# Kernel optimization log

Hardware: AMD Instinct MI355X
Metric: run time of the kernel (lower is better)

Reference implementation:

```python
import jax, jax.numpy as jnp
import numpy as np
import math

B, S, H, NH = 2, 2048, 1024, 16
DK = H // NH
EPS = 1e-5

def setup_inputs() -> dict:
    key = jax.random.key(0)
    ks = jax.random.split(key, 8)
    sd = 0.02
    return {
        "x": jax.random.normal(ks[0], (B, S, H), dtype=jnp.float32),
        "ln1_w": jnp.ones((H,), jnp.float32),
        "ln1_b": jnp.zeros((H,), jnp.float32),
        "W_qkv": jax.random.normal(ks[1], (H, 3 * H), jnp.float32) * sd,
        "b_qkv": jnp.zeros((3 * H,), jnp.float32),
        "W_o": jax.random.normal(ks[2], (H, H), jnp.float32) * sd,
        "b_o": jnp.zeros((H,), jnp.float32),
        "ln2_w": jnp.ones((H,), jnp.float32),
        "ln2_b": jnp.zeros((H,), jnp.float32),
        "W_fc": jax.random.normal(ks[3], (H, 4 * H), jnp.float32) * sd,
        "b_fc": jnp.zeros((4 * H,), jnp.float32),
        "W_proj": jax.random.normal(ks[4], (4 * H, H), jnp.float32) * sd,
        "b_proj": jnp.zeros((H,), jnp.float32),
    }

def _layernorm(x, w, b):
    mu = jnp.mean(x, axis=-1, keepdims=True)
    var = jnp.mean(jnp.square(x - mu), axis=-1, keepdims=True)
    return (x - mu) * jax.lax.rsqrt(var + EPS) * w + b

def _attn(x, W_qkv, b_qkv, W_o, b_o):
    bs, seq, _ = x.shape
    qkv = x @ W_qkv + b_qkv                      # [b,s,3H]
    q, k, v = jnp.split(qkv, 3, axis=-1)
    q = q.reshape(bs, seq, NH, DK).transpose(0, 2, 1, 3)  # [b,h,s,d]
    k = k.reshape(bs, seq, NH, DK).transpose(0, 2, 1, 3)
    v = v.reshape(bs, seq, NH, DK).transpose(0, 2, 1, 3)
    scores = jnp.einsum("bhqd,bhkd->bhqk", q, k) / math.sqrt(DK)
    causal = jnp.tril(jnp.ones((seq, seq), bool))
    scores = jnp.where(causal, scores, -jnp.inf)
    attn = jax.nn.softmax(scores, axis=-1)
    out = jnp.einsum("bhqk,bhkd->bhqd", attn, v)
    out = out.transpose(0, 2, 1, 3).reshape(bs, seq, H)
    return out @ W_o + b_o

def reference(x, ln1_w, ln1_b, W_qkv, b_qkv, W_o, b_o, ln2_w, ln2_b, W_fc, b_fc, W_proj, b_proj):
    x = x + _attn(_layernorm(x, ln1_w, ln1_b), W_qkv, b_qkv, W_o, b_o)
    h = _layernorm(x, ln2_w, ln2_b)
    h = jax.nn.gelu(h @ W_fc + b_fc, approximate=False) @ W_proj + b_proj
    return x + h
```

## Files before the change

### kernel.cpp

```cpp
#include <hip/hip_runtime.h>
#include <hip/hip_bf16.h>
#include <math.h>

#define H_DIM 1024
#define SEQ   2048
#define BATCH 2
#define NHEAD 16
#define DKV   64
#define ROWS  (BATCH*SEQ)
#define QSCALE 0.18033688f

typedef __attribute__((ext_vector_type(8))) short short8;
typedef __attribute__((ext_vector_type(4))) float f32x4;

static __device__ __forceinline__ unsigned short f32_bf16(float f) {
    unsigned int u = __builtin_bit_cast(unsigned int, f);
    u += 0x7FFF + ((u >> 16) & 1);
    return (unsigned short)(u >> 16);
}
static __device__ __forceinline__ float bf16_f32(unsigned short h) {
    return __builtin_bit_cast(float, (unsigned int)h << 16);
}

static __device__ __forceinline__ float fast_erf(float x) {
    float ax = fabsf(x);
    float t = 1.0f / fmaf(0.3275911f, ax, 1.0f);
    float p = t * fmaf(t, fmaf(t, fmaf(t, fmaf(t, 1.061405429f, -1.453152027f),
                                       1.421413741f), -0.284496736f), 0.254829592f);
    float y = fmaf(-p, __expf(-ax * ax), 1.0f);
    return copysignf(y, x);
}

static __device__ __forceinline__ void gload16(const unsigned short* g, unsigned short* l) {
    __builtin_amdgcn_global_load_lds(
        (const __attribute__((address_space(1))) void*)g,
        (__attribute__((address_space(3))) void*)l,
        16, 0, 0);
}

__global__ __launch_bounds__(256) void transpose_bf16(const float* __restrict__ in,
                                                      unsigned short* __restrict__ out,
                                                      int K, int N) {
    __shared__ float tile[32][33];
    int n0 = blockIdx.x * 32, k0 = blockIdx.y * 32;
    int tx = threadIdx.x & 31, ty = threadIdx.x >> 5;
    #pragma unroll
    for (int i = 0; i < 4; ++i)
        tile[ty + i * 8][tx] = in[(size_t)(k0 + ty + i * 8) * N + n0 + tx];
    __syncthreads();
    #pragma unroll
    for (int i = 0; i < 4; ++i)
        out[(size_t)(n0 + ty + i * 8) * K + k0 + tx] = f32_bf16(tile[tx][ty + i * 8]);
}

template<int BF16IN>
__global__ __launch_bounds__(256) void ln_any(const void* __restrict__ xin,
                                              const float* __restrict__ w,
                                              const float* __restrict__ bb,
                                              unsigned short* __restrict__ out) {
    int row = blockIdx.x;
    int tid = threadIdx.x;
    float4 v;
    if (BF16IN) {
        ushort4 u = ((const ushort4*)((const unsigned short*)xin + (size_t)row * H_DIM))[tid];
        v.x = bf16_f32(u.x); v.y = bf16_f32(u.y); v.z = bf16_f32(u.z); v.w = bf16_f32(u.w);
    } else {
        v = ((const float4*)((const float*)xin + (size_t)row * H_DIM))[tid];
    }
    float s  = v.x + v.y + v.z + v.w;
    float s2 = v.x*v.x + v.y*v.y + v.z*v.z + v.w*v.w;
    #pragma unroll
    for (int off = 1; off < 64; off <<= 1) {
        s  += __shfl_xor(s,  off, 64);
        s2 += __shfl_xor(s2, off, 64);
    }
    __shared__ float red[8];
    int wv = tid >> 6;
    if ((tid & 63) == 0) { red[wv] = s; red[4 + wv] = s2; }
    __syncthreads();
    s  = red[0] + red[1] + red[2] + red[3];
    s2 = red[4] + red[5] + red[6] + red[7];
    float mu = s * (1.0f / H_DIM);
    float rs = rsqrtf(s2 * (1.0f / H_DIM) - mu * mu + 1e-5f);
    float4 wv4 = ((const float4*)w)[tid];
    float4 bv4 = ((const float4*)bb)[tid];
    ushort4 o;
    o.x = f32_bf16((v.x - mu) * rs * wv4.x + bv4.x);
    o.y = f32_bf16((v.y - mu) * rs * wv4.y + bv4.y);
    o.z = f32_bf16((v.z - mu) * rs * wv4.z + bv4.z);
    o.w = f32_bf16((v.w - mu) * rs * wv4.w + bv4.w);
    ((ushort4*)(out + (size_t)row * H_DIM))[tid] = o;
}

template<int EPI>
static __device__ __forceinline__ void epi_store(f32x4 a, int row0, int col, int N,
                                                 const float* __restrict__ bias,
                                                 const float* __restrict__ resid,
                                                 float* __restrict__ outF,
                                                 unsigned short* __restrict__ outH,
                                                 unsigned short* __restrict__ outH2) {
    float bv = bias[col];
    if (EPI == 4 && col >= 2048) {
        int bb = row0 >> 11, ss = row0 & 2047;
        int hd = col - 2048;
        ushort4 u;
        u.x = f32_bf16(a[0] + bv);
        u.y = f32_bf16(a[1] + bv);
        u.z = f32_bf16(a[2] + bv);
        u.w = f32_bf16(a[3] + bv);
        *(ushort4*)&outH2[((size_t)bb * 1024 + hd) * SEQ + ss] = u;
    } else {
        #pragma unroll
        for (int j = 0; j < 4; ++j) {
            int row = row0 + j;
            size_t idx = (size_t)row * N + col;
            float c = a[j] + bv;
            if (EPI == 0) {
                outF[idx] = c;
            } else if (EPI == 1) {
                outF[idx] = resid[idx] + c;
            } else if (EPI == 2) {
                float g = 0.5f * c * (1.0f + fast_erf(c * 0.70710678118f));
                outH[idx] = f32_bf16(g);
            } else if (EPI == 3) {
                outH[idx] = f32_bf16(c);
            } else if (EPI == 5) {
                outH[idx] = f32_bf16(resid[idx] + c);
            } else if (EPI == 6) {
                outF[idx] = bf16_f32(outH2[idx]) + c;
            } else {
                float c2 = (col < 1024) ? c * QSCALE : c;
                outH[(size_t)row * 2048 + col] = f32_bf16(c2);
            }
        }
    }
}

template<int EPI, int NI>
__global__ __launch_bounds__(512) void gemmT(const unsigned short* __restrict__ A,
                                             const unsigned short* __restrict__ Bt,
                                             const float* __restrict__ bias,
                                             const float* __restrict__ resid,
                                             float* __restrict__ outF,
                                             unsigned short* __restrict__ outH,
                                             unsigned short* __restrict__ outH2,
                                             int gx, int N, int K) {
    constexpr int BN = NI * 32;
    constexpr int WN = BN / 4;
    constexpr int NT = WN / 16;
    __shared__ __attribute__((aligned(16))) unsigned short As[128][64];
    __shared__ __attribute__((aligned(16))) unsigned short Bs[BN][64];
    int tid = threadIdx.x;
    int w = tid >> 6, l = tid & 63;
    int l15 = l & 15, lg = l >> 4;
    int wm = w & 1, wn = w >> 1;

    int qq = gridDim.x >> 3;
    int wg = (blockIdx.x & 7) * qq + (blockIdx.x >> 3);
    int bm = wg / gx, bn = wg - bm * gx;
    int m0 = bm * 128, n0 = bn * BN;

    f32x4 acc[4][NT] = {};

    const unsigned short* aptr[2];
    unsigned short* lA[2];
    #pragma unroll
    for (int j = 0; j < 2; ++j) {
        int slot = j * 512 + tid;
        int row = slot >> 3;
        int lchunk = (slot & 7) ^ (row & 7);
        aptr[j] = A + (size_t)(m0 + row) * K + lchunk * 8;
        lA[j] = &As[0][0] + (size_t)slot * 8 - l * 8;
    }
    const unsigned short* bptr[NI / 2];
    unsigned short* lB[NI / 2];
    #pragma unroll
    for (int j = 0; j < NI / 2; ++j) {
        int slot = j * 512 + tid;
        int row = slot >> 3;
        int lchunk = (slot & 7) ^ (row & 7);
        bptr[j] = Bt + (size_t)(n0 + row) * K + lchunk * 8;
        lB[j] = &Bs[0][0] + (size_t)slot * 8 - l * 8;
    }
    int swz[2];
    swz[0] = ((0 + lg) ^ (l15 & 7)) * 8;
    swz[1] = ((4 + lg) ^ (l15 & 7)) * 8;
    const unsigned short* pA = &As[wm * 64 + l15][0];
    const unsigned short* pB = &Bs[wn * WN + l15][0];

    for (int k0 = 0; k0 < K; k0 += 64) {
        __syncthreads();
        #pragma unroll
        for (int j = 0; j < 2; ++j) gload16(aptr[j] + k0, lA[j]);
        #pragma unroll
        for (int j = 0; j < NI / 2; ++j) gload16(bptr[j] + k0, lB[j]);
        __syncthreads();

        #pragma unroll
        for (int ks = 0; ks < 2; ++ks) {
            short8 af[4], bf[NT];
            #pragma unroll
            for (int mi = 0; mi < 4; ++mi)
                af[mi] = *(const short8*)(pA + mi * 16 * 64 + swz[ks]);
            #pragma unroll
            for (int ni = 0; ni < NT; ++ni)
                bf[ni] = *(const short8*)(pB + ni * 16 * 64 + swz[ks]);
            #pragma unroll
            for (int mi = 0; mi < 4; ++mi)
                #pragma unroll
                for (int ni = 0; ni < NT; ++ni)
                    acc[mi][ni] = __builtin_amdgcn_mfma_f32_16x16x32_bf16(af[mi], bf[ni], acc[mi][ni], 0, 0, 0);
        }
    }

    #pragma unroll
    for (int mi = 0; mi < 4; ++mi)
        #pragma unroll
        for (int ni = 0; ni < NT; ++ni)
            epi_store<EPI>(acc[mi][ni], m0 + wm * 64 + mi * 16 + lg * 4,
                           n0 + wn * WN + ni * 16 + l15, N, bias, resid, outF, outH, outH2);
}

__global__ __launch_bounds__(512) void attn_mfma(const unsigned short* __restrict__ qk,
                                                 const unsigned short* __restrict__ vT,
                                                 unsigned short* __restrict__ out) {
    int bid = blockIdx.x;
    int swz = (bid & 7) * 64 + (bid >> 3);
    int b  = swz >> 8;
    int h  = (swz >> 4) & 15;
    int qt = 15 - (swz & 15);
    int tid = threadIdx.x;
    int w = tid >> 6, l = tid & 63;
    int l15 = l & 15, lg = l >> 4;

    __shared__ __attribute__((aligned(16))) unsigned short Ks[2][64][64];
    __shared__ __attribute__((aligned(16))) unsigned short Vt[2][64][64];
    __shared__ __attribute__((aligned(16))) unsigned short Ps[8][16][72];

    int qrow = qt * 128 + w * 16 + l15;
    short8 qf[2];
    {
        const unsigned short* qp = qk + (size_t)(b * SEQ + qrow) * 2048 + h * DKV + lg * 8;
        qf[0] = *(const short8*)qp;
        qf[1] = *(const short8*)(qp + 32);
    }
    short8 vf5;
    #pragma unroll
    for (int i = 0; i < 8; ++i) vf5[i] = (l15 == 0) ? (short)0x3F80 : (short)0;

    int srow = tid >> 3;
    int scl  = (tid & 7) * 8;
    int spc  = (((tid & 7) ^ (srow & 7)) * 8);
    const unsigned short* kbase = qk + (size_t)(b * SEQ + srow) * 2048 + 1024 + h * DKV + scl;
    const unsigned short* vbase = vT + ((size_t)(b * NHEAD + h) * DKV + srow) * SEQ + scl;

    int rk0 = ((0 * 4 + lg) ^ (l15 & 7)) * 8;
    int rk1 = ((1 * 4 + lg) ^ (l15 & 7)) * 8;

    float m = -1e30f;
    f32x4 oacc[4] = {};
    f32x4 oext = {};

    int nt = 2 * qt + 2;

    short8 kr0 = *(const short8*)kbase;
    short8 vr0 = *(const short8*)vbase;
    *(short8*)&Ks[0][srow][spc] = kr0;
    *(short8*)&Vt[0][srow][spc] = vr0;
    short8 kr1 = *(const short8*)(kbase + (size_t)64 * 2048);
    short8 vr1 = *(const short8*)(vbase + 64);
    __syncthreads();

#define ATTN_COMPUTE(BUF, KT)                                                          \
    {                                                                                  \
        f32x4 sc[4] = {};                                                              \
        __builtin_amdgcn_s_setprio(1);                                                 \
        _Pragma("unroll")                                                              \
        for (int st = 0; st < 4; ++st) {                                               \
            short8 kf0 = *(const short8*)&Ks[BUF][st * 16 + l15][rk0];                 \
            sc[st] = __builtin_amdgcn_mfma_f32_16x16x32_bf16(kf0, qf[0], sc[st], 0, 0, 0); \
            short8 kf1 = *(const short8*)&Ks[BUF][st * 16 + l15][rk1];                 \
            sc[st] = __builtin_amdgcn_mfma_f32_16x16x32_bf16(kf1, qf[1], sc[st], 0, 0, 0); \
        }                                                                              \
        __builtin_amdgcn_s_setprio(0);                                                 \
        float pv[4][4];                                                                \
        float pmax = -1e30f;                                                           \
        bool needmask = ((KT) * 64 + 63) > (qt * 128 + w * 16);      \
        if (needmask) {                                                                \
            int klim = qrow - (KT) * 64;                                               \
            _Pragma("unroll")                                                          \
            for (int st = 0; st < 4; ++st) {                                           \
                _Pragma("unroll")                                                      \
                for (int j = 0; j < 4; ++j) {                                          \
                    float s = sc[st][j];                                               \
                    if (st * 16 + lg * 4 + j > klim) s = -1e30f;                       \
                    pv[st][j] = s;                                                     \
                    pmax = fmaxf(pmax, s);                                             \
                }                                                                      \
            }                                                                          \
        } else {                                                                       \
            _Pragma("unroll")                                                          \
            for (int st = 0; st < 4; ++st) {                                           \
                _Pragma("unroll")                                                      \
                for (int j = 0; j < 4; ++j) {                                          \
                    pv[st][j] = sc[st][j];                                             \
                    pmax = fmaxf(pmax, sc[st][j]);                                     \
                }                                                                      \
            }                                                                          \
        }                                                                              \
        if (!__all(pmax - m <= 8.0f)) {                                                \
            float pr = fmaxf(pmax, __shfl_xor(pmax, 16, 64));                          \
            pr = fmaxf(pr, __shfl_xor(pr, 32, 64));                                    \
            float mn = fmaxf(m, pr);                                                   \
            float scl2 = exp2f(m - mn);                                                \
            _Pragma("unroll")                                                          \
            for (int d = 0; d < 4; ++d)                                                \
                _Pragma("unroll")                                                      \
                for (int j = 0; j < 4; ++j)                                            \
                    oacc[d][j] *= scl2;                                                \
            _Pragma("unroll")                                                          \
            for (int j = 0; j < 4; ++j) oext[j] *= scl2;                               \
            m = mn;                                                                    \
        }                                                                              \
        _Pragma("unroll")                                                              \
        for (int st = 0; st < 4; ++st) {                                               \
            float p0 = exp2f(pv[st][0] - m);                                           \
            float p1 = exp2f(pv[st][1] - m);                                           \
            float p2 = exp2f(pv[st][2] - m);                                           \
            float p3 = exp2f(pv[st][3] - m);                                           \
            unsigned int ua, ub;                                                       \
            asm("v_cvt_pk_bf16_f32 %0, %1, %2" : "=v"(ua) : "v"(p0), "v"(p1));         \
            asm("v_cvt_pk_bf16_f32 %0, %1, %2" : "=v"(ub) : "v"(p2), "v"(p3));         \
            uint2 u = make_uint2(ua, ub);                                              \
            *(uint2*)&Ps[w][l15][st * 16 + lg * 4] = u;                                \
        }                                                                              \
        __builtin_amdgcn_s_setprio(1);                                                 \
        _Pragma("unroll")                                                              \
        for (int ks = 0; ks < 2; ++ks) {                                               \
            short8 pf = *(const short8*)&Ps[w][l15][ks * 32 + lg * 8];                 \
            int rv = (ks == 0) ? rk0 : rk1;                                            \
            _Pragma("unroll")                                                          \
            for (int d = 0; d < 4; ++d) {                                              \
                short8 vf = *(const short8*)&Vt[BUF][d * 16 + l15][rv];                \
                oacc[d] = __builtin_amdgcn_mfma_f32_16x16x32_bf16(vf, pf, oacc[d], 0, 0, 0); \
            }                                                                          \
            oext = __builtin_amdgcn_mfma_f32_16x16x32_bf16(vf5, pf, oext, 0, 0, 0);    \
        }                                                                              \
        __builtin_amdgcn_s_setprio(0);                                                 \
    }

    for (int t = 0; t < nt; t += 2) {
        *(short8*)&Ks[1][srow][spc] = kr1;
        *(short8*)&Vt[1][srow][spc] = vr1;
        if (t + 2 < nt) {
            kr0 = *(const short8*)(kbase + (size_t)(t + 2) * 64 * 2048);
            vr0 = *(const short8*)(vbase + (t + 2) * 64);
        }
        ATTN_COMPUTE(0, t);
        __syncthreads();
        if (t + 2 < nt) {
            *(short8*)&Ks[0][srow][spc] = kr0;
            *(short8*)&Vt[0][srow][spc] = vr0;
            kr1 = *(const short8*)(kbase + (size_t)(t + 3) * 64 * 2048);
            vr1 = *(const short8*)(vbase + (t + 3) * 64);
        }
        ATTN_COMPUTE(1, t + 1);
        __syncthreads();
    }
#undef ATTN_COMPUTE

    float lsum = __shfl(oext[0], l15, 64);
    float inv = 1.0f / lsum;
    size_t ob = (size_t)(b * SEQ + qrow) * H_DIM + h * DKV;
    #pragma unroll
    for (int d = 0; d < 4; ++d) {
        ushort4 u;
        #pragma unroll
        for (int j = 0; j < 4; ++j)
            ((unsigned short*)&u)[j] = f32_bf16(oacc[d][j] * inv);
        *(ushort4*)&out[ob + d * 16 + lg * 4] = u;
    }
}

extern "C" void kernel_launch(void* const* d_in, const int* in_sizes, int n_in,
                              void* d_out, int out_size, void* d_ws, size_t ws_size,
                              hipStream_t stream) {
    const float* x     = (const float*)d_in[0];
    const float* ln1w  = (const float*)d_in[1];
    const float* ln1b  = (const float*)d_in[2];
    const float* Wqkv  = (const float*)d_in[3];
    const float* bqkv  = (const float*)d_in[4];
    const float* Wo    = (const float*)d_in[5];
    const float* bo    = (const float*)d_in[6];
    const float* ln2w  = (const float*)d_in[7];
    const float* ln2b  = (const float*)d_in[8];
    const float* Wfc   = (const float*)d_in[9];
    const float* bfc   = (const float*)d_in[10];
    const float* Wproj = (const float*)d_in[11];
    const float* bproj = (const float*)d_in[12];
    float* out = (float*)d_out;

    char* ws = (char*)d_ws;
    size_t off = 0;
    auto take = [&](size_t bytes) {
        void* p = ws + off;
        off += (bytes + 255) & ~(size_t)255;
        return p;
    };

    unsigned short* WqT  = (unsigned short*)take((size_t)3072 * 1024 * 2);
    unsigned short* WoT  = (unsigned short*)take((size_t)1024 * 1024 * 2);
    unsigned short* WfcT = (unsigned short*)take((size_t)4096 * 1024 * 2);
    unsigned short* WpT  = (unsigned short*)take((size_t)1024 * 4096 * 2);
    unsigned short* xn1   = (unsigned short*)take((size_t)ROWS * 1024 * 2);
    unsigned short* qk_h  = (unsigned short*)take((size_t)ROWS * 2048 * 2);
    unsigned short* vT    = (unsigned short*)take((size_t)ROWS * 1024 * 2);
    unsigned short* attn  = (unsigned short*)take((size_t)ROWS * 1024 * 2);
    unsigned short* x1h   = (unsigned short*)take((size_t)ROWS * 1024 * 2);
    unsigned short* xn2   = (unsigned short*)take((size_t)ROWS * 1024 * 2);
    unsigned short* hbuf  = (unsigned short*)take((size_t)ROWS * 4096 * 2);

    transpose_bf16<<<dim3(3072 / 32, 1024 / 32), 256, 0, stream>>>(Wqkv,  WqT,  1024, 3072);
    transpose_bf16<<<dim3(1024 / 32, 1024 / 32), 256, 0, stream>>>(Wo,    WoT,  1024, 1024);
    transpose_bf16<<<dim3(4096 / 32, 1024 / 32), 256, 0, stream>>>(Wfc,   WfcT, 1024, 4096);
    transpose_bf16<<<dim3(1024 / 32, 4096 / 32), 256, 0, stream>>>(Wproj, WpT,  4096, 1024);

    ln_any<0><<<ROWS, 256, 0, stream>>>(x, ln1w, ln1b, xn1);

    gemmT<4, 4><<<768, 512, 0, stream>>>(xn1, WqT, bqkv, nullptr, nullptr, qk_h, vT, 24, 3072, 1024);

    attn_mfma<<<512, 512, 0, stream>>>(qk_h, vT, attn);

    gemmT<5, 2><<<512, 512, 0, stream>>>(attn, WoT, bo, x, nullptr, x1h, nullptr, 16, 1024, 1024);

    ln_any<1><<<ROWS, 256, 0, stream>>>(x1h, ln2w, ln2b, xn2);

    gemmT<2, 4><<<1024, 512, 0, stream>>>(xn2, WfcT, bfc, nullptr, nullptr, hbuf, nullptr, 32, 4096, 1024);

    gemmT<6, 2><<<512, 512, 0, stream>>>(hbuf, WpT, bproj, nullptr, out, nullptr, x1h, 16, 1024, 4096);
}
```

Baseline: 238.1 us.

## Pair causal query tiles per attention block and remap GEMM tiles per XCD

The attention kernel now uses 256 threads and gives each block two 64-row query tiles, one from the top and one from the bottom of the causal triangle. Both tiles share each loaded K/V tile, so every block does the same amount of work and K/V reuse goes up. The GEMM block-to-tile mapping now gives each of the 8 XCDs a contiguous rectangle of output tiles, meant to improve L2 reuse of A and B. The costs are more register pressure from two accumulator sets and a per-tile barrier on a double buffer.

```diff
diff --git a/kernel.cpp b/kernel.cpp
--- a/kernel.cpp
+++ b/kernel.cpp
@@ -144,7 +144,7 @@
                                              float* __restrict__ outF,
                                              unsigned short* __restrict__ outH,
                                              unsigned short* __restrict__ outH2,
-                                             int gx, int N, int K) {
+                                             int cm, int cn, int ncc, int N, int K) {
     constexpr int BN = NI * 32;
     constexpr int WN = BN / 4;
     constexpr int NT = WN / 16;
@@ -155,9 +155,11 @@
     int l15 = l & 15, lg = l >> 4;
     int wm = w & 1, wn = w >> 1;
 
-    int qq = gridDim.x >> 3;
-    int wg = (blockIdx.x & 7) * qq + (blockIdx.x >> 3);
-    int bm = wg / gx, bn = wg - bm * gx;
+    int c = blockIdx.x & 7, lwg = blockIdx.x >> 3;
+    int lm = lwg / cn, ln = lwg - lm * cn;
+    int ccr = c / ncc;
+    int bm = ccr * cm + lm;
+    int bn = (c - ccr * ncc) * cn + ln;
     int m0 = bm * 128, n0 = bn * BN;
 
     f32x4 acc[4][NT] = {};
@@ -221,73 +223,73 @@
                            n0 + wn * WN + ni * 16 + l15, N, bias, resid, outF, outH, outH2);
 }
 
-__global__ __launch_bounds__(512) void attn_mfma(const unsigned short* __restrict__ qk,
+__global__ __launch_bounds__(256) void attn_mfma(const unsigned short* __restrict__ qk,
                                                  const unsigned short* __restrict__ vT,
                                                  unsigned short* __restrict__ out) {
     int bid = blockIdx.x;
     int swz = (bid & 7) * 64 + (bid >> 3);
     int b  = swz >> 8;
     int h  = (swz >> 4) & 15;
-    int qt = 15 - (swz & 15);
+    int p  = swz & 15;
     int tid = threadIdx.x;
     int w = tid >> 6, l = tid & 63;
     int l15 = l & 15, lg = l >> 4;
 
     __shared__ __attribute__((aligned(16))) unsigned short Ks[2][64][64];
     __shared__ __attribute__((aligned(16))) unsigned short Vt[2][64][64];
-    __shared__ __attribute__((aligned(16))) unsigned short Ps[8][16][72];
-
-    int qrow = qt * 128 + w * 16 + l15;
-    short8 qf[2];
+    __shared__ __attribute__((aligned(16))) unsigned short Ps[4][16][72];
+
+    short8 vf5;
+    #pragma unroll
+    for (int i = 0; i < 8; ++i) vf5[i] = (l15 == 0) ? (short)0x3F80 : (short)0;
+
+    int sr = tid >> 2;
+    int c0 = (tid & 3) * 2, c1 = c0 + 1;
+    int sp0 = ((c0 ^ (sr & 7)) * 8);
+    int sp1 = ((c1 ^ (sr & 7)) * 8);
+    const unsigned short* kb0 = qk + (size_t)(b * SEQ + sr) * 2048 + 1024 + h * DKV + c0 * 8;
+    const unsigned short* kb1 = kb0 + 8;
+    const unsigned short* vb0 = vT + ((size_t)(b * NHEAD + h) * DKV + sr) * SEQ + c0 * 8;
+    const unsigned short* vb1 = vb0 + 8;
+
+    int rk0 = ((0 + lg) ^ (l15 & 7)) * 8;
+    int rk1 = ((4 + lg) ^ (l15 & 7)) * 8;
+
+    int qhi = 31 - p, qlo = p;
+    int qrow_h = qhi * 64 + w * 16 + l15;
+    int qrow_l = qlo * 64 + w * 16 + l15;
+    short8 qf0_h, qf1_h, qf0_l, qf1_l;
     {
-        const unsigned short* qp = qk + (size_t)(b * SEQ + qrow) * 2048 + h * DKV + lg * 8;
-        qf[0] = *(const short8*)qp;
-        qf[1] = *(const short8*)(qp + 32);
-    }
-    short8 vf5;
-    #pragma unroll
-    for (int i = 0; i < 8; ++i) vf5[i] = (l15 == 0) ? (short)0x3F80 : (short)0;
-
-    int srow = tid >> 3;
-    int scl  = (tid & 7) * 8;
-    int spc  = (((tid & 7) ^ (srow & 7)) * 8);
-    const unsigned short* kbase = qk + (size_t)(b * SEQ + srow) * 2048 + 1024 + h * DKV + scl;
-    const unsigned short* vbase = vT + ((size_t)(b * NHEAD + h) * DKV + srow) * SEQ + scl;
-
-    int rk0 = ((0 * 4 + lg) ^ (l15 & 7)) * 8;
-    int rk1 = ((1 * 4 + lg) ^ (l15 & 7)) * 8;
-
-    float m = -1e30f;
-    f32x4 oacc[4] = {};
-    f32x4 oext = {};
-
-    int nt = 2 * qt + 2;
-
-    short8 kr0 = *(const short8*)kbase;
-    short8 vr0 = *(const short8*)vbase;
-    *(short8*)&Ks[0][srow][spc] = kr0;
-    *(short8*)&Vt[0][srow][spc] = vr0;
-    short8 kr1 = *(const short8*)(kbase + (size_t)64 * 2048);
-    short8 vr1 = *(const short8*)(vbase + 64);
-    __syncthreads();
-
-#define ATTN_COMPUTE(BUF, KT)                                                          \
+        const unsigned short* qp = qk + (size_t)(b * SEQ + qrow_h) * 2048 + h * DKV + lg * 8;
+        qf0_h = *(const short8*)qp;
+        qf1_h = *(const short8*)(qp + 32);
+        qp = qk + (size_t)(b * SEQ + qrow_l) * 2048 + h * DKV + lg * 8;
+        qf0_l = *(const short8*)qp;
+        qf1_l = *(const short8*)(qp + 32);
+    }
+
+    float m_h = -1e30f, m_l = -1e30f;
+    f32x4 oacc_h[4] = {}, oacc_l[4] = {};
+    f32x4 oext_h = {}, oext_l = {};
+
+    int NTL = qhi + 1;
+
+#define ATTN_TILE(SUF, BU, DOMASK, KLIM)                                               \
     {                                                                                  \
         f32x4 sc[4] = {};                                                              \
         __builtin_amdgcn_s_setprio(1);                                                 \
         _Pragma("unroll")                                                              \
         for (int st = 0; st < 4; ++st) {                                               \
-            short8 kf0 = *(const short8*)&Ks[BUF][st * 16 + l15][rk0];                 \
-            sc[st] = __builtin_amdgcn_mfma_f32_16x16x32_bf16(kf0, qf[0], sc[st], 0, 0, 0); \
-            short8 kf1 = *(const short8*)&Ks[BUF][st * 16 + l15][rk1];                 \
-            sc[st] = __builtin_amdgcn_mfma_f32_16x16x32_bf16(kf1, qf[1], sc[st], 0, 0, 0); \
+            short8 kf0 = *(const short8*)&Ks[BU][st * 16 + l15][rk0];                  \
+            sc[st] = __builtin_amdgcn_mfma_f32_16x16x32_bf16(kf0, qf0_##SUF, sc[st], 0, 0, 0); \
+            short8 kf1 = *(const short8*)&Ks[BU][st * 16 + l15][rk1];                  \
+            sc[st] = __builtin_amdgcn_mfma_f32_16x16x32_bf16(kf1, qf1_##SUF, sc[st], 0, 0, 0); \
         }                                                                              \
         __builtin_amdgcn_s_setprio(0);                                                 \
         float pv[4][4];                                                                \
         float pmax = -1e30f;                                                           \
-        bool needmask = ((KT) * 64 + 63) > (qt * 128 + w * 16);      \
-        if (needmask) {                                                                \
-            int klim = qrow - (KT) * 64;                                               \
+        if (DOMASK) {                                                                  \
+            int klim = (KLIM);                                                         \
             _Pragma("unroll")                                                          \
             for (int st = 0; st < 4; ++st) {                                           \
                 _Pragma("unroll")                                                      \
@@ -308,26 +310,26 @@
                 }                                                                      \
             }                                                                          \
         }                                                                              \
-        if (!__all(pmax - m <= 8.0f)) {                                                \
+        if (!__all(pmax - m_##SUF <= 8.0f)) {                                          \
             float pr = fmaxf(pmax, __shfl_xor(pmax, 16, 64));                          \
             pr = fmaxf(pr, __shfl_xor(pr, 32, 64));                                    \
-            float mn = fmaxf(m, pr);                                                   \
-            float scl2 = exp2f(m - mn);                                                \
+            float mn = fmaxf(m_##SUF, pr);                                             \
+            float scl2 = exp2f(m_##SUF - mn);                                          \
             _Pragma("unroll")                                                          \
             for (int d = 0; d < 4; ++d)                                                \
                 _Pragma("unroll")                                                      \
                 for (int j = 0; j < 4; ++j)                                            \
-                    oacc[d][j] *= scl2;                                                \
+                    oacc_##SUF[d][j] *= scl2;                                          \
             _Pragma("unroll")                                                          \
-            for (int j = 0; j < 4; ++j) oext[j] *= scl2;                               \
-            m = mn;                                                                    \
+            for (int j = 0; j < 4; ++j) oext_##SUF[j] *= scl2;                         \
+            m_##SUF = mn;                                                              \
         }                                                                              \
         _Pragma("unroll")                                                              \
         for (int st = 0; st < 4; ++st) {                                               \
-            float p0 = exp2f(pv[st][0] - m);                                           \
-            float p1 = exp2f(pv[st][1] - m);                                           \
-            float p2 = exp2f(pv[st][2] - m);                                           \
-            float p3 = exp2f(pv[st][3] - m);                                           \
+            float p0 = exp2f(pv[st][0] - m_##SUF);                                     \
+            float p1 = exp2f(pv[st][1] - m_##SUF);                                     \
+            float p2 = exp2f(pv[st][2] - m_##SUF);                                     \
+            float p3 = exp2f(pv[st][3] - m_##SUF);                                     \
             unsigned int ua, ub;                                                       \
             asm("v_cvt_pk_bf16_f32 %0, %1, %2" : "=v"(ua) : "v"(p0), "v"(p1));         \
             asm("v_cvt_pk_bf16_f32 %0, %1, %2" : "=v"(ub) : "v"(p2), "v"(p3));         \
@@ -341,44 +343,81 @@
             int rv = (ks == 0) ? rk0 : rk1;                                            \
             _Pragma("unroll")                                                          \
             for (int d = 0; d < 4; ++d) {                                              \
-                short8 vf = *(const short8*)&Vt[BUF][d * 16 + l15][rv];                \
-                oacc[d] = __builtin_amdgcn_mfma_f32_16x16x32_bf16(vf, pf, oacc[d], 0, 0, 0); \
+                short8 vf = *(const short8*)&Vt[BU][d * 16 + l15][rv];                 \
+                oacc_##SUF[d] = __builtin_amdgcn_mfma_f32_16x16x32_bf16(vf, pf, oacc_##SUF[d], 0, 0, 0); \
             }                                                                          \
-            oext = __builtin_amdgcn_mfma_f32_16x16x32_bf16(vf5, pf, oext, 0, 0, 0);    \
+            oext_##SUF = __builtin_amdgcn_mfma_f32_16x16x32_bf16(vf5, pf, oext_##SUF, 0, 0, 0); \
         }                                                                              \
         __builtin_amdgcn_s_setprio(0);                                                 \
     }
 
-    for (int t = 0; t < nt; t += 2) {
-        *(short8*)&Ks[1][srow][spc] = kr1;
-        *(short8*)&Vt[1][srow][spc] = vr1;
-        if (t + 2 < nt) {
-            kr0 = *(const short8*)(kbase + (size_t)(t + 2) * 64 * 2048);
-            vr0 = *(const short8*)(vbase + (t + 2) * 64);
-        }
-        ATTN_COMPUTE(0, t);
+    short8 kr0 = *(const short8*)kb0;
+    short8 kr1 = *(const short8*)kb1;
+    short8 vr0 = *(const short8*)vb0;
+    short8 vr1 = *(const short8*)vb1;
+    *(short8*)&Ks[0][sr][sp0] = kr0;
+    *(short8*)&Ks[0][sr][sp1] = kr1;
+    *(short8*)&Vt[0][sr][sp0] = vr0;
+    *(short8*)&Vt[0][sr][sp1] = vr1;
+    if (NTL > 1) {
+        kr0 = *(const short8*)(kb0 + (size_t)64 * 2048);
+        kr1 = *(const short8*)(kb1 + (size_t)64 * 2048);
+        vr0 = *(const short8*)(vb0 + 64);
+        vr1 = *(const short8*)(vb1 + 64);
+    }
+    __syncthreads();
+
+    for (int t = 0; t < NTL; ++t) {
+        int nb = (t + 1) & 1;
+        if (t + 1 < NTL) {
+            *(short8*)&Ks[nb][sr][sp0] = kr0;
+            *(short8*)&Ks[nb][sr][sp1] = kr1;
+            *(short8*)&Vt[nb][sr][sp0] = vr0;
+            *(short8*)&Vt[nb][sr][sp1] = vr1;
+            if (t + 2 < NTL) {
+                kr0 = *(const short8*)(kb0 + (size_t)(t + 2) * 64 * 2048);
+                kr1 = *(const short8*)(kb1 + (size_t)(t + 2) * 64 * 2048);
+                vr0 = *(const short8*)(vb0 + (t + 2) * 64);
+                vr1 = *(const short8*)(vb1 + (t + 2) * 64);
+            }
+        }
+        int bu = t & 1;
+
+        ATTN_TILE(h, bu, (t == qhi), qrow_h - t * 64);
+        if (t <= qlo) {
+            ATTN_TILE(l, bu, (t == qlo), qrow_l - t * 64);
+        }
         __syncthreads();
-        if (t + 2 < nt) {
-            *(short8*)&Ks[0][srow][spc] = kr0;
-            *(short8*)&Vt[0][srow][spc] = vr0;
-            kr1 = *(const short8*)(kbase + (size_t)(t + 3) * 64 * 2048);
-            vr1 = *(const short8*)(vbase + (t + 3) * 64);
-        }
-        ATTN_COMPUTE(1, t + 1);
-        __syncthreads();
-    }
-#undef ATTN_COMPUTE
-
-    float lsum = __shfl(oext[0], l15, 64);
-    float inv = 1.0f / lsum;
-    size_t ob = (size_t)(b * SEQ + qrow) * H_DIM + h * DKV;
-    #pragma unroll
-    for (int d = 0; d < 4; ++d) {
-        ushort4 u;
-        #pragma unroll
-        for (int j = 0; j < 4; ++j)
-            ((unsigned short*)&u)[j] = f32_bf16(oacc[d][j] * inv);
-        *(ushort4*)&out[ob + d * 16 + lg * 4] = u;
+    }
+#undef ATTN_TILE
+
+    {
+        float lsum = __shfl(oext_h[0], l15, 64);
+        float inv = 1.0f / lsum;
+        size_t ob = (size_t)(b * SEQ + qrow_h) * H_DIM + h * DKV;
+        #pragma unroll
+        for (int d = 0; d < 4; ++d) {
+            float o0 = oacc_h[d][0] * inv, o1 = oacc_h[d][1] * inv;
+            float o2 = oacc_h[d][2] * inv, o3 = oacc_h[d][3] * inv;
+            unsigned int ua, ub;
+            asm("v_cvt_pk_bf16_f32 %0, %1, %2" : "=v"(ua) : "v"(o0), "v"(o1));
+            asm("v_cvt_pk_bf16_f32 %0, %1, %2" : "=v"(ub) : "v"(o2), "v"(o3));
+            *(uint2*)&out[ob + d * 16 + lg * 4] = make_uint2(ua, ub);
+        }
+    }
+    {
+        float lsum = __shfl(oext_l[0], l15, 64);
+        float inv = 1.0f / lsum;
+        size_t ob = (size_t)(b * SEQ + qrow_l) * H_DIM + h * DKV;
+        #pragma unroll
+        for (int d = 0; d < 4; ++d) {
+            float o0 = oacc_l[d][0] * inv, o1 = oacc_l[d][1] * inv;
+            float o2 = oacc_l[d][2] * inv, o3 = oacc_l[d][3] * inv;
+            unsigned int ua, ub;
+            asm("v_cvt_pk_bf16_f32 %0, %1, %2" : "=v"(ua) : "v"(o0), "v"(o1));
+            asm("v_cvt_pk_bf16_f32 %0, %1, %2" : "=v"(ub) : "v"(o2), "v"(o3));
+            *(uint2*)&out[ob + d * 16 + lg * 4] = make_uint2(ua, ub);
+        }
     }
 }
 
@@ -427,15 +466,15 @@
 
     ln_any<0><<<ROWS, 256, 0, stream>>>(x, ln1w, ln1b, xn1);
 
-    gemmT<4, 4><<<768, 512, 0, stream>>>(xn1, WqT, bqkv, nullptr, nullptr, qk_h, vT, 24, 3072, 1024);
-
-    attn_mfma<<<512, 512, 0, stream>>>(qk_h, vT, attn);
-
-    gemmT<5, 2><<<512, 512, 0, stream>>>(attn, WoT, bo, x, nullptr, x1h, nullptr, 16, 1024, 1024);
+    gemmT<4, 4><<<768, 512, 0, stream>>>(xn1, WqT, bqkv, nullptr, nullptr, qk_h, vT, 8, 12, 2, 3072, 1024);
+
+    attn_mfma<<<512, 256, 0, stream>>>(qk_h, vT, attn);
+
+    gemmT<5, 2><<<512, 512, 0, stream>>>(attn, WoT, bo, x, nullptr, x1h, nullptr, 4, 16, 1, 1024, 1024);
 
     ln_any<1><<<ROWS, 256, 0, stream>>>(x1h, ln2w, ln2b, xn2);
 
-    gemmT<2, 4><<<1024, 512, 0, stream>>>(xn2, WfcT, bfc, nullptr, nullptr, hbuf, nullptr, 32, 4096, 1024);
-
-    gemmT<6, 2><<<512, 512, 0, stream>>>(hbuf, WpT, bproj, nullptr, out, nullptr, x1h, 16, 1024, 4096);
-}
+    gemmT<2, 4><<<1024, 512, 0, stream>>>(xn2, WfcT, bfc, nullptr, nullptr, hbuf, nullptr, 8, 16, 2, 4096, 1024);
+
+    gemmT<6, 2><<<512, 512, 0, stream>>>(hbuf, WpT, bproj, nullptr, out, nullptr, x1h, 4, 16, 1, 1024, 4096);
+}
```

After: 225.5 us. 5.3% less time.
